# Optimization experiments

Measured on AMD Instinct MI355X. Metric: run time of the kernel, lower is better.

Reference implementation:

```python
import jax, jax.numpy as jnp
import numpy as np

NUM_HEADS = 16


def setup_inputs() -> dict:
    key = jax.random.key(0)
    ks = jax.random.split(key, 5)
    B, S, D = 2, 2048, 1024
    x = jax.random.normal(ks[0], (B, S, D), dtype=jnp.float32)
    # torch Linear weights are [out_features, in_features]; y = x @ W.T + b
    Wq = jax.random.normal(ks[1], (D, D), dtype=jnp.float32) * (D ** -0.5)
    Wk = jax.random.normal(ks[2], (D, D), dtype=jnp.float32) * (D ** -0.5)
    Wv = jax.random.normal(ks[3], (D, D), dtype=jnp.float32) * (D ** -0.5)
    Wo = jax.random.normal(ks[4], (D, D), dtype=jnp.float32) * (D ** -0.5)
    bo = jnp.zeros((D,), dtype=jnp.float32)
    return {"x": x, "Wq": Wq, "Wk": Wk, "Wv": Wv, "Wo": Wo, "bo": bo}


def reference(x, Wq, Wk, Wv, Wo, bo):
    B, S, D = x.shape
    H = NUM_HEADS
    dh = D // H
    # projections (torch Linear: x @ W.T)
    q = (x @ Wq.T).reshape(B, S, H, dh).transpose(0, 2, 1, 3)  # [B,H,S,dh]
    k = (x @ Wk.T).reshape(B, S, H, dh).transpose(0, 2, 1, 3)
    v = (x @ Wv.T).reshape(B, S, H, dh).transpose(0, 2, 1, 3)
    # NOTE: original code takes shape[-1] of the TRANSPOSED key (n,H,dh,S),
    # so the softmax scale is seq_length**-0.5 (a bug we reproduce faithfully).
    scale = jnp.asarray(S, x.dtype) ** -0.5
    scores = jnp.einsum("bhqd,bhkd->bhqk", q, k)  # [B,H,S,S]
    causal = jnp.triu(jnp.ones((S, S), dtype=bool), k=1)
    scores = jnp.where(causal, -jnp.inf, scores * scale)
    weights = jax.nn.softmax(scores, axis=-1)
    # dropout p=0.0 -> identity
    ctx = jnp.einsum("bhqk,bhkd->bhqd", weights, v)  # [B,H,S,dh]
    ctx = ctx.transpose(0, 2, 1, 3).reshape(B, S, D)
    return ctx @ Wo.T + bo
```

## Files before the change

kernel.cpp:

```cpp
#include <hip/hip_runtime.h>
#include <hip/hip_bf16.h>

#define B_SZ    2
#define S_LEN   2048
#define D_MODEL 1024
#define H_NUM   16
#define DH      64
#define M_TOT   (B_SZ * S_LEN)

#define QSCALE (0.022097086912079608f * 1.4426950408889634f)

typedef __attribute__((ext_vector_type(8)))  short          bf16x8;
typedef __attribute__((ext_vector_type(4)))  float          f32x4;
typedef __attribute__((ext_vector_type(16))) float          f32x16;
typedef __attribute__((ext_vector_type(8)))  unsigned short u16x8;
typedef __attribute__((ext_vector_type(4)))  unsigned short u16x4;

__device__ inline unsigned short f2bf(float f) {
  unsigned int u = __float_as_uint(f);
  u += 0x7fffu + ((u >> 16) & 1u);
  return (unsigned short)(u >> 16);
}

__device__ inline float bf2f(unsigned short u) {
  return __uint_as_float(((unsigned)u) << 16);
}

__device__ inline float fexp2(float x) {
#if __has_builtin(__builtin_amdgcn_exp2f)
  return __builtin_amdgcn_exp2f(x);
#else
  return exp2f(x);
#endif
}

__device__ inline unsigned cvt_pk_bf16(float lo, float hi) {
  unsigned r;
  asm("v_cvt_pk_bf16_f32 %0, %1, %2" : "=v"(r) : "v"(lo), "v"(hi));
  return r;
}

__device__ inline void gload16(const void* g, void* l) {
  __builtin_amdgcn_global_load_lds(
      (const __attribute__((address_space(1))) void*)g,
      (__attribute__((address_space(3))) void*)l, 16, 0, 0);
}

__global__ __launch_bounds__(256) void to_bf16_all(
    const float* __restrict__ x, const float* __restrict__ wq,
    const float* __restrict__ wk, const float* __restrict__ wv,
    const float* __restrict__ wo, unsigned short* __restrict__ xb,
    unsigned short* __restrict__ wqb, unsigned short* __restrict__ wkb,
    unsigned short* __restrict__ wvb, unsigned short* __restrict__ wob) {
  const size_t i = ((size_t)blockIdx.x * 256 + threadIdx.x) * 8;
  const float* src;
  unsigned short* dst;
  size_t off;
  if (i < 4194304)      { src = x;  dst = xb;  off = i; }
  else if (i < 5242880) { src = wq; dst = wqb; off = i - 4194304; }
  else if (i < 6291456) { src = wk; dst = wkb; off = i - 5242880; }
  else if (i < 7340032) { src = wv; dst = wvb; off = i - 6291456; }
  else                  { src = wo; dst = wob; off = i - 7340032; }
  f32x4 a = *(const f32x4*)(src + off);
  f32x4 b = *(const f32x4*)(src + off + 4);
  u16x8 o;
#pragma unroll
  for (int j = 0; j < 4; j++) { o[j] = f2bf(a[j]); o[4 + j] = f2bf(b[j]); }
  *(u16x8*)(dst + off) = o;
}

__device__ __forceinline__ void gemm_core(const unsigned short* __restrict__ A,
                                          const unsigned short* __restrict__ W,
                                          unsigned short (*Al)[128][32],
                                          unsigned short (*Bl)[128][32],
                                          int mbase, int nbase,
                                          f32x4 acc[4][4]) {
  const int tid  = threadIdx.x;
  const int lane = tid & 63;
  const int wid  = tid >> 6;
  const int wr   = wid >> 1, wc = wid & 1;
  const int g    = lane >> 4, lr = lane & 15;

  const int r0 = tid >> 2;
  const int cg = (tid & 3) ^ ((tid >> 3) & 3);

  const unsigned short* Abase = A + (size_t)(mbase + r0) * D_MODEL + cg * 8;
  const unsigned short* Wbase = W + (size_t)(nbase + r0) * D_MODEL + cg * 8;
  char* ldsA0 = (char*)Al + wid * 1024;
  char* ldsB0 = (char*)Bl + wid * 1024;

  gload16(Abase, ldsA0);
  gload16(Abase + (size_t)64 * D_MODEL, ldsA0 + 4096);
  gload16(Wbase, ldsB0);
  gload16(Wbase + (size_t)64 * D_MODEL, ldsB0 + 4096);
  gload16(Abase + 32, ldsA0 + 8192);
  gload16(Abase + (size_t)64 * D_MODEL + 32, ldsA0 + 8192 + 4096);
  gload16(Wbase + 32, ldsB0 + 8192);
  gload16(Wbase + (size_t)64 * D_MODEL + 32, ldsB0 + 8192 + 4096);

  const int NKT = D_MODEL / 32;
  int cur = 0, nx2 = 2;
  for (int kt = 0; kt < NKT; ++kt) {
    if (kt + 2 < NKT) {
      const unsigned short* As = Abase + (kt + 2) * 32;
      const unsigned short* Ws = Wbase + (kt + 2) * 32;
      char* la = ldsA0 + nx2 * 8192;
      char* lb = ldsB0 + nx2 * 8192;
      gload16(As, la);
      gload16(As + (size_t)64 * D_MODEL, la + 4096);
      gload16(Ws, lb);
      gload16(Ws + (size_t)64 * D_MODEL, lb + 4096);
      asm volatile("s_waitcnt vmcnt(8)" ::: "memory");
    } else if (kt + 1 < NKT) {
      asm volatile("s_waitcnt vmcnt(4)" ::: "memory");
    } else {
      asm volatile("s_waitcnt vmcnt(0)" ::: "memory");
    }
    __builtin_amdgcn_s_barrier();

    bf16x8 af[4], bfr[4];
#pragma unroll
    for (int i = 0; i < 4; i++) {
      const int ra = wr * 64 + i * 16 + lr;
      af[i] = *(const bf16x8*)&Al[cur][ra][(g ^ ((ra >> 1) & 3)) * 8];
      const int rb = wc * 64 + i * 16 + lr;
      bfr[i] = *(const bf16x8*)&Bl[cur][rb][(g ^ ((rb >> 1) & 3)) * 8];
    }
    __builtin_amdgcn_s_setprio(1);
#pragma unroll
    for (int i = 0; i < 4; i++)
#pragma unroll
      for (int j = 0; j < 4; j++)
        acc[i][j] = __builtin_amdgcn_mfma_f32_16x16x32_bf16(af[i], bfr[j],
                                                            acc[i][j], 0, 0, 0);
    __builtin_amdgcn_s_setprio(0);
    asm volatile("" ::: "memory");
    __builtin_amdgcn_s_barrier();
    cur = (cur == 2) ? 0 : cur + 1;
    nx2 = (nx2 == 2) ? 0 : nx2 + 1;
  }
}

__global__ __launch_bounds__(256) void gemm_qkv(
    const unsigned short* __restrict__ xb, const unsigned short* __restrict__ wqb,
    const unsigned short* __restrict__ wkb, const unsigned short* __restrict__ wvb,
    unsigned short* __restrict__ qb, unsigned short* __restrict__ kb,
    unsigned short* __restrict__ vt) {
  __shared__ unsigned short Al[3][128][32];
  __shared__ unsigned short Bl[3][128][32];
  const int lin = blockIdx.x;
  const int w8  = (lin & 7) * 96 + (lin >> 3);
  const int xq  = w8 & 7;
  const int yq  = (w8 >> 3) & 31;
  const int z   = w8 >> 8;
  const unsigned short* W = (z == 0) ? wqb : (z == 1) ? wkb : wvb;
  unsigned short* dst = (z == 0) ? qb : (z == 1) ? kb : vt;
  const float sc = (z == 0) ? QSCALE : 1.0f;

  f32x4 acc[4][4];
#pragma unroll
  for (int i = 0; i < 4; i++)
#pragma unroll
    for (int j = 0; j < 4; j++) acc[i][j] = (f32x4){0.f, 0.f, 0.f, 0.f};

  const int mbase = yq * 128, nbase = xq * 128;
  gemm_core(xb, W, Al, Bl, mbase, nbase, acc);

  const int lane = threadIdx.x & 63, wid = threadIdx.x >> 6;
  const int wr = wid >> 1, wc = wid & 1, g = lane >> 4, lr = lane & 15;
#pragma unroll
  for (int i = 0; i < 4; i++) {
#pragma unroll
    for (int j = 0; j < 4; j++) {
      const int mg0 = mbase + wr * 64 + i * 16 + g * 4;
      const int ng  = nbase + wc * 64 + j * 16 + lr;
      if (z < 2) {
#pragma unroll
        for (int r = 0; r < 4; r++)
          dst[(size_t)(mg0 + r) * D_MODEL + ng] = f2bf(acc[i][j][r] * sc);
      } else {
        const int hh = ng >> 6, dd = ng & 63;
        const int bb = mg0 >> 11, ss = mg0 & 2047;
        u16x4 pk;
#pragma unroll
        for (int r = 0; r < 4; r++) pk[r] = f2bf(acc[i][j][r]);
        *(u16x4*)&dst[((size_t)((bb * H_NUM + hh) * DH + dd)) * S_LEN + ss] = pk;
      }
    }
  }
}

__global__ __launch_bounds__(256) void gemm_out(
    const unsigned short* __restrict__ cx, const unsigned short* __restrict__ wob,
    float* __restrict__ out, const float* __restrict__ bo) {
  __shared__ unsigned short Al[3][128][32];
  __shared__ unsigned short Bl[3][128][32];
  const int lin = blockIdx.x;
  const int w8  = (lin & 7) * 32 + (lin >> 3);
  const int xq  = w8 & 7;
  const int yq  = w8 >> 3;
  f32x4 acc[4][4];
#pragma unroll
  for (int i = 0; i < 4; i++)
#pragma unroll
    for (int j = 0; j < 4; j++) acc[i][j] = (f32x4){0.f, 0.f, 0.f, 0.f};

  const int mbase = yq * 128, nbase = xq * 128;
  gemm_core(cx, wob, Al, Bl, mbase, nbase, acc);

  const int lane = threadIdx.x & 63, wid = threadIdx.x >> 6;
  const int wr = wid >> 1, wc = wid & 1, g = lane >> 4, lr = lane & 15;
#pragma unroll
  for (int i = 0; i < 4; i++) {
#pragma unroll
    for (int j = 0; j < 4; j++) {
      const int mg0 = mbase + wr * 64 + i * 16 + g * 4;
      const int ng  = nbase + wc * 64 + j * 16 + lr;
      const float bv = bo[ng];
#pragma unroll
      for (int r = 0; r < 4; r++)
        out[(size_t)(mg0 + r) * D_MODEL + ng] = acc[i][j][r] + bv;
    }
  }
}

#define ENT(qi, k0, k1, p) ((unsigned)(qi) | ((unsigned)(k0) << 8) | \
                            ((unsigned)(k1) << 16) | ((unsigned)(p) << 24))
__device__ const unsigned att_sched[40] = {
    ENT(3, 0, 8, 0),   ENT(7, 0, 8, 0),   ENT(7, 8, 16, 1),
    ENT(10, 0, 8, 0),  ENT(11, 0, 8, 0),  ENT(11, 8, 16, 1),
    ENT(11, 16, 24, 2),ENT(14, 0, 8, 0),  ENT(14, 15, 23, 2),
    ENT(15, 0, 8, 0),  ENT(15, 8, 16, 1), ENT(15, 16, 24, 2),
    ENT(15, 24, 32, 3),
    ENT(6, 0, 7, 0),   ENT(6, 7, 14, 1),  ENT(9, 0, 7, 0),
    ENT(9, 7, 14, 1),  ENT(10, 8, 15, 1), ENT(10, 15, 22, 2),
    ENT(12, 0, 7, 0),  ENT(12, 13, 20, 2),ENT(13, 0, 7, 0),
    ENT(13, 7, 14, 1), ENT(13, 14, 21, 2),ENT(13, 21, 28, 3),
    ENT(14, 8, 15, 1), ENT(14, 23, 30, 3),
    ENT(2, 0, 6, 0),   ENT(5, 0, 6, 0),   ENT(5, 6, 12, 1),
    ENT(8, 0, 6, 0),   ENT(8, 6, 12, 1),  ENT(8, 12, 18, 2),
    ENT(9, 14, 20, 2), ENT(12, 7, 13, 1), ENT(12, 20, 26, 3),
    ENT(4, 0, 5, 0),   ENT(4, 5, 10, 1),  ENT(1, 0, 4, 0),
    ENT(0, 0, 2, 0),
};
__device__ const int att_chunks[16]   = {1,1,1,1, 2,2,2,2, 3,3,3,3, 4,4,4,4};
__device__ const int att_mlbase[16]   = {0,1,2,3, 4,6,8,10, 12,15,18,21,
                                         24,28,32,36};
__device__ const int att_opbase[16]   = {0,0,0,0, 0,1,2,3, 4,6,8,10,
                                         12,15,18,21};

__global__ __launch_bounds__(256) void attn_v8(
    const unsigned short* __restrict__ qb, const unsigned short* __restrict__ kb,
    const unsigned short* __restrict__ vt, unsigned short* __restrict__ cx,
    unsigned short* __restrict__ Opart, float* __restrict__ ml) {
  __shared__ alignas(16) char smem[65536];

  const int tid  = threadIdx.x;
  const int lane = tid & 63;
  const int w    = tid >> 6;
  const int hi   = lane >> 5;
  const int lq   = lane & 31;
  const int bid  = blockIdx.x;

  const unsigned ent = att_sched[bid >> 5];
  const int qi   = ent & 255;
  const int kt0  = (ent >> 8) & 255;
  const int kt1  = (ent >> 16) & 255;
  const int part = (ent >> 24) & 255;
  const int nch  = att_chunks[qi];
  const int bh   = bid & 31;
  const int b    = bh >> 4, h = bh & 15;

  const int qg0  = qi * 128 + w * 32;
  const int tok0 = b * S_LEN + qg0;

  const int sr  = tid >> 3;
  const int scg = (tid & 7) ^ (sr & 7);
  const unsigned short* kbase =
      kb + (size_t)(b * S_LEN) * D_MODEL + h * DH + scg * 8;
  const unsigned short* vrow =
      vt + ((size_t)((b * H_NUM + h) * DH + sr)) * S_LEN + scg * 8;
  char* ldsK0 = smem + w * 1024;
  char* ldsV0 = smem + 32768 + w * 1024;

  bf16x8 qf[4];
  {
    const unsigned short* qrow =
        qb + (size_t)(tok0 + lq) * D_MODEL + h * DH + hi * 8;
#pragma unroll
    for (int ks = 0; ks < 4; ks++) qf[ks] = *(const bf16x8*)(qrow + ks * 16);
  }

  f32x16 ctx0, ctx1;
#pragma unroll
  for (int r = 0; r < 16; r++) { ctx0[r] = 0.f; ctx1[r] = 0.f; }
  float l_run = 0.f;

  const int ndiag = 2 * qi;

  {
    const unsigned short* sK = kbase + (size_t)(kt0 * 64 + sr) * D_MODEL;
    gload16(sK, ldsK0);
    gload16(sK + (size_t)32 * D_MODEL, ldsK0 + 4096);
    const unsigned short* sV = vrow + kt0 * 64;
    gload16(sV, ldsV0);
    gload16(sV + (size_t)32 * S_LEN, ldsV0 + 4096);
    if (kt0 + 1 < kt1) {
      const unsigned short* sK1 = sK + (size_t)64 * D_MODEL;
      gload16(sK1, ldsK0 + 8192);
      gload16(sK1 + (size_t)32 * D_MODEL, ldsK0 + 8192 + 4096);
      const unsigned short* sV1 = sV + 64;
      gload16(sV1, ldsV0 + 8192);
      gload16(sV1 + (size_t)32 * S_LEN, ldsV0 + 8192 + 4096);
    }
  }

  int cur = 0, nx2 = 2;
  for (int kt = kt0; kt < kt1; ++kt) {
    if (kt + 2 < kt1) {
      const unsigned short* sK = kbase + (size_t)((kt + 2) * 64 + sr) * D_MODEL;
      gload16(sK, ldsK0 + nx2 * 8192);
      gload16(sK + (size_t)32 * D_MODEL, ldsK0 + nx2 * 8192 + 4096);
      const unsigned short* sV = vrow + (kt + 2) * 64;
      gload16(sV, ldsV0 + nx2 * 8192);
      gload16(sV + (size_t)32 * S_LEN, ldsV0 + nx2 * 8192 + 4096);
      asm volatile("s_waitcnt vmcnt(8)" ::: "memory");
    } else if (kt + 1 < kt1) {
      asm volatile("s_waitcnt vmcnt(4)" ::: "memory");
    } else {
      asm volatile("s_waitcnt vmcnt(0)" ::: "memory");
    }
    __builtin_amdgcn_s_barrier();

    const char* Kc = smem + cur * 8192;
    const char* Vc = smem + 32768 + cur * 8192;

    f32x16 s0, s1;
#pragma unroll
    for (int r = 0; r < 16; r++) { s0[r] = 0.f; s1[r] = 0.f; }
    __builtin_amdgcn_s_setprio(1);
#pragma unroll
    for (int ks = 0; ks < 4; ks++) {
      const int c = ((ks * 2 + hi) ^ (lq & 7)) * 16;
      bf16x8 k0 = *(const bf16x8*)(Kc + lq * 128 + c);
      bf16x8 k1 = *(const bf16x8*)(Kc + (32 + lq) * 128 + c);
      s0 = __builtin_amdgcn_mfma_f32_32x32x16_bf16(k0, qf[ks], s0, 0, 0, 0);
      s1 = __builtin_amdgcn_mfma_f32_32x32x16_bf16(k1, qf[ks], s1, 0, 0, 0);
    }
    __builtin_amdgcn_s_setprio(0);

    if (kt >= ndiag) {
      const int relq = qg0 + lq - kt * 64 - 4 * hi;
#pragma unroll
      for (int r = 0; r < 16; r++) {
        const int ko = (r & 3) + 8 * (r >> 2);
        s0[r] = (ko > relq) ? -1e30f : s0[r];
        s1[r] = (ko + 32 > relq) ? -1e30f : s1[r];
      }
    }

    float lsAcc[4];
#pragma unroll
    for (int ks = 0; ks < 4; ks++) {
      float p[8];
#pragma unroll
      for (int j = 0; j < 8; j++) {
        const int r = (ks & 1) * 8 + j;
        const float sv = (ks < 2) ? s0[r] : s1[r];
        p[j] = fexp2(sv);
      }
      lsAcc[ks] = ((p[0] + p[1]) + (p[2] + p[3])) +
                  ((p[4] + p[5]) + (p[6] + p[7]));
      unsigned a0 = cvt_pk_bf16(p[0], p[1]);
      unsigned a1 = cvt_pk_bf16(p[4], p[5]);
      unsigned b0 = cvt_pk_bf16(p[2], p[3]);
      unsigned b1 = cvt_pk_bf16(p[6], p[7]);
      asm("v_permlane32_swap_b32 %0, %1" : "+v"(a0), "+v"(a1));
      asm("v_permlane32_swap_b32 %0, %1" : "+v"(b0), "+v"(b1));
      union { unsigned u[4]; bf16x8 v; } pw;
      pw.u[0] = a0;
      pw.u[1] = b0;
      pw.u[2] = a1;
      pw.u[3] = b1;
      const int c = ((ks * 2 + hi) ^ (lq & 7)) * 16;
      bf16x8 v0 = *(const bf16x8*)(Vc + lq * 128 + c);
      bf16x8 v1 = *(const bf16x8*)(Vc + (32 + lq) * 128 + c);
      __builtin_amdgcn_s_setprio(1);
      ctx0 = __builtin_amdgcn_mfma_f32_32x32x16_bf16(v0, pw.v, ctx0, 0, 0, 0);
      ctx1 = __builtin_amdgcn_mfma_f32_32x32x16_bf16(v1, pw.v, ctx1, 0, 0, 0);
      __builtin_amdgcn_s_setprio(0);
    }
    l_run += (lsAcc[0] + lsAcc[1]) + (lsAcc[2] + lsAcc[3]);
    cur = (cur + 1) & 3;
    nx2 = (nx2 + 1) & 3;
  }

  __builtin_amdgcn_s_barrier();
  unsigned short (*Tl)[32][72] = (unsigned short (*)[32][72])smem;
  const float lfull = l_run + __shfl_xor(l_run, 32);
  const float inv   = (nch == 1) ? (1.0f / lfull) : 1.0f;
#pragma unroll
  for (int rp = 0; rp < 8; rp++) {
    const int r  = rp * 2;
    const int d0 = (r & 3) + 8 * (r >> 2) + 4 * hi;
    *(unsigned*)&Tl[w][lq][d0] = cvt_pk_bf16(ctx0[r] * inv, ctx0[r + 1] * inv);
    *(unsigned*)&Tl[w][lq][32 + d0] =
        cvt_pk_bf16(ctx1[r] * inv, ctx1[r + 1] * inv);
  }
  asm volatile("s_waitcnt lgkmcnt(0)" ::: "memory");
  const int q2 = lane >> 1;
  unsigned short* dstp;
  if (nch == 1 || part == 0) {
    dstp = &cx[(size_t)(tok0 + q2) * D_MODEL + h * DH];
  } else {
    dstp = Opart + ((size_t)((att_opbase[qi] + part - 1) * 32 + bh) * 128 +
                    w * 32 + q2) * 64;
  }
#pragma unroll
  for (int i = 0; i < 4; i++) {
    const int ch = (lane & 1) * 4 + i;
    u16x8 vv = *(const u16x8*)&Tl[w][q2][ch * 8];
    *(u16x8*)&dstp[ch * 8] = vv;
  }
  if (nch > 1 && hi == 0) {
    float2 v2 = make_float2(0.0f, lfull);
    *(float2*)&ml[((size_t)((att_mlbase[qi] + part) * 32 + bh) * 128 +
                   w * 32 + lq) * 2] = v2;
  }
}

__global__ __launch_bounds__(256) void attn_combine(
    const unsigned short* __restrict__ Opart, const float* __restrict__ ml,
    unsigned short* __restrict__ cx) {
  const int gid = blockIdx.x * 256 + threadIdx.x;
  const int sub = gid & 7;
  const int row = (gid >> 3) & 127;
  const int bh  = (gid >> 10) & 31;
  const int qi  = 4 + (gid >> 15);
  const int nch = att_chunks[qi];
  const int b = bh >> 4, h = bh & 15;
  const int tok = b * S_LEN + qi * 128 + row;

  float mv[4], lv[4];
  float m = -1e30f;
#pragma unroll 4
  for (int p = 0; p < 4; p++) {
    if (p < nch) {
      const size_t mi =
          ((size_t)((att_mlbase[qi] + p) * 32 + bh) * 128 + row) * 2;
      mv[p] = ml[mi];
      lv[p] = ml[mi + 1];
      m = fmaxf(m, mv[p]);
    }
  }
  float denom = 0.f;
  float wgt[4];
#pragma unroll 4
  for (int p = 0; p < 4; p++) {
    if (p < nch) {
      wgt[p] = fexp2(mv[p] - m);
      denom += lv[p] * wgt[p];
    }
  }
  const float inv = 1.0f / denom;

  float acc[8];
  {
    u16x8 a = *(const u16x8*)&cx[(size_t)tok * D_MODEL + h * DH + sub * 8];
#pragma unroll
    for (int j = 0; j < 8; j++) acc[j] = bf2f(a[j]) * wgt[0];
  }
#pragma unroll 4
  for (int p = 1; p < 4; p++) {
    if (p < nch) {
      const unsigned short* src =
          Opart + ((size_t)((att_opbase[qi] + p - 1) * 32 + bh) * 128 + row) * 64;
      u16x8 a = *(const u16x8*)&src[sub * 8];
#pragma unroll
      for (int j = 0; j < 8; j++) acc[j] += bf2f(a[j]) * wgt[p];
    }
  }
  u16x8 o;
#pragma unroll
  for (int j = 0; j < 8; j++) o[j] = f2bf(acc[j] * inv);
  *(u16x8*)&cx[(size_t)tok * D_MODEL + h * DH + sub * 8] = o;
}

extern "C" void kernel_launch(void* const* d_in, const int* in_sizes, int n_in,
                              void* d_out, int out_size, void* d_ws,
                              size_t ws_size, hipStream_t stream) {
  const float* x  = (const float*)d_in[0];
  const float* Wq = (const float*)d_in[1];
  const float* Wk = (const float*)d_in[2];
  const float* Wv = (const float*)d_in[3];
  const float* Wo = (const float*)d_in[4];
  const float* bo = (const float*)d_in[5];
  float* out = (float*)d_out;

  unsigned short* xb  = (unsigned short*)d_ws;
  unsigned short* wqb = xb  + (size_t)M_TOT * D_MODEL;
  unsigned short* wkb = wqb + (size_t)D_MODEL * D_MODEL;
  unsigned short* wvb = wkb + (size_t)D_MODEL * D_MODEL;
  unsigned short* wob = wvb + (size_t)D_MODEL * D_MODEL;
  unsigned short* qb  = wob + (size_t)D_MODEL * D_MODEL;
  unsigned short* kb  = qb  + (size_t)M_TOT * D_MODEL;
  unsigned short* vt  = kb  + (size_t)M_TOT * D_MODEL;
  unsigned short* cx  = vt  + (size_t)M_TOT * D_MODEL;
  unsigned short* Opart = xb;
  float*          ml    = (float*)(xb + (size_t)768 * 8192);

  to_bf16_all<<<4096, 256, 0, stream>>>(x, Wq, Wk, Wv, Wo, xb, wqb, wkb, wvb,
                                        wob);
  gemm_qkv<<<dim3(768), 256, 0, stream>>>(xb, wqb, wkb, wvb, qb, kb, vt);
  attn_v8<<<dim3(1280), 256, 0, stream>>>(qb, kb, vt, cx, Opart, ml);
  attn_combine<<<dim3(1536), 256, 0, stream>>>(Opart, ml, cx);
  gemm_out<<<dim3(256), 256, 0, stream>>>(cx, wob, out, bo);
}
```

Baseline: 109.8 us.

## Widen attention blocks to 256 queries with 8 waves sharing K/V tiles

The attention kernel now processes 256 query rows per block using 512 threads (8 waves), up from 128 rows with 4 waves. Each staged K/V tile is therefore reused by twice as many waves, halving redundant global K/V loads. The split-K work schedule, chunk tables, per-wave diagonal index and the partial-output and ml buffer layouts are rebuilt for 256-row tiles. The combine kernel drops its exp2 max-rescaling, since the stored max is always zero, and simply sums partials and denominators. In exchange the grid shrinks to 640 larger blocks, which may leave compute units less evenly loaded and lowers occupancy per block.

```diff
diff --git a/kernel.cpp b/kernel.cpp
--- a/kernel.cpp
+++ b/kernel.cpp
@@ -226,30 +226,21 @@
 
 #define ENT(qi, k0, k1, p) ((unsigned)(qi) | ((unsigned)(k0) << 8) | \
                             ((unsigned)(k1) << 16) | ((unsigned)(p) << 24))
-__device__ const unsigned att_sched[40] = {
-    ENT(3, 0, 8, 0),   ENT(7, 0, 8, 0),   ENT(7, 8, 16, 1),
-    ENT(10, 0, 8, 0),  ENT(11, 0, 8, 0),  ENT(11, 8, 16, 1),
-    ENT(11, 16, 24, 2),ENT(14, 0, 8, 0),  ENT(14, 15, 23, 2),
-    ENT(15, 0, 8, 0),  ENT(15, 8, 16, 1), ENT(15, 16, 24, 2),
-    ENT(15, 24, 32, 3),
-    ENT(6, 0, 7, 0),   ENT(6, 7, 14, 1),  ENT(9, 0, 7, 0),
-    ENT(9, 7, 14, 1),  ENT(10, 8, 15, 1), ENT(10, 15, 22, 2),
-    ENT(12, 0, 7, 0),  ENT(12, 13, 20, 2),ENT(13, 0, 7, 0),
-    ENT(13, 7, 14, 1), ENT(13, 14, 21, 2),ENT(13, 21, 28, 3),
-    ENT(14, 8, 15, 1), ENT(14, 23, 30, 3),
-    ENT(2, 0, 6, 0),   ENT(5, 0, 6, 0),   ENT(5, 6, 12, 1),
-    ENT(8, 0, 6, 0),   ENT(8, 6, 12, 1),  ENT(8, 12, 18, 2),
-    ENT(9, 14, 20, 2), ENT(12, 7, 13, 1), ENT(12, 20, 26, 3),
-    ENT(4, 0, 5, 0),   ENT(4, 5, 10, 1),  ENT(1, 0, 4, 0),
-    ENT(0, 0, 2, 0),
+__device__ const unsigned att_sched[20] = {
+    ENT(1, 0, 8, 0),
+    ENT(3, 0, 8, 0),  ENT(3, 8, 16, 1),
+    ENT(5, 0, 8, 0),  ENT(5, 8, 16, 1),  ENT(5, 16, 24, 2),
+    ENT(7, 0, 8, 0),  ENT(7, 8, 16, 1),  ENT(7, 16, 24, 2), ENT(7, 24, 32, 3),
+    ENT(4, 0, 7, 0),  ENT(4, 7, 14, 1),
+    ENT(6, 0, 7, 0),  ENT(6, 7, 14, 1),  ENT(6, 14, 21, 2), ENT(6, 21, 28, 3),
+    ENT(2, 0, 6, 0),  ENT(2, 6, 12, 1),  ENT(4, 14, 20, 2),
+    ENT(0, 0, 4, 0),
 };
-__device__ const int att_chunks[16]   = {1,1,1,1, 2,2,2,2, 3,3,3,3, 4,4,4,4};
-__device__ const int att_mlbase[16]   = {0,1,2,3, 4,6,8,10, 12,15,18,21,
-                                         24,28,32,36};
-__device__ const int att_opbase[16]   = {0,0,0,0, 0,1,2,3, 4,6,8,10,
-                                         12,15,18,21};
-
-__global__ __launch_bounds__(256) void attn_v8(
+__device__ const int att_chunks[8] = {1, 1, 2, 2, 3, 3, 4, 4};
+__device__ const int att_mlbase[8] = {0, 1, 2, 4, 6, 9, 12, 16};
+__device__ const int att_opbase[8] = {0, 0, 0, 1, 2, 4, 6, 9};
+
+__global__ __launch_bounds__(512) void attn_v9(
     const unsigned short* __restrict__ qb, const unsigned short* __restrict__ kb,
     const unsigned short* __restrict__ vt, unsigned short* __restrict__ cx,
     unsigned short* __restrict__ Opart, float* __restrict__ ml) {
@@ -271,7 +262,7 @@
   const int bh   = bid & 31;
   const int b    = bh >> 4, h = bh & 15;
 
-  const int qg0  = qi * 128 + w * 32;
+  const int qg0  = qi * 256 + w * 32;
   const int tok0 = b * S_LEN + qg0;
 
   const int sr  = tid >> 3;
@@ -296,37 +287,24 @@
   for (int r = 0; r < 16; r++) { ctx0[r] = 0.f; ctx1[r] = 0.f; }
   float l_run = 0.f;
 
-  const int ndiag = 2 * qi;
+  const int ndiag = 4 * qi + (w >> 1);
 
   {
-    const unsigned short* sK = kbase + (size_t)(kt0 * 64 + sr) * D_MODEL;
-    gload16(sK, ldsK0);
-    gload16(sK + (size_t)32 * D_MODEL, ldsK0 + 4096);
-    const unsigned short* sV = vrow + kt0 * 64;
-    gload16(sV, ldsV0);
-    gload16(sV + (size_t)32 * S_LEN, ldsV0 + 4096);
-    if (kt0 + 1 < kt1) {
-      const unsigned short* sK1 = sK + (size_t)64 * D_MODEL;
-      gload16(sK1, ldsK0 + 8192);
-      gload16(sK1 + (size_t)32 * D_MODEL, ldsK0 + 8192 + 4096);
-      const unsigned short* sV1 = sV + 64;
-      gload16(sV1, ldsV0 + 8192);
-      gload16(sV1 + (size_t)32 * S_LEN, ldsV0 + 8192 + 4096);
-    }
+    gload16(kbase + (size_t)(kt0 * 64 + sr) * D_MODEL, ldsK0);
+    gload16(vrow + kt0 * 64, ldsV0);
+    gload16(kbase + (size_t)((kt0 + 1) * 64 + sr) * D_MODEL, ldsK0 + 8192);
+    gload16(vrow + (kt0 + 1) * 64, ldsV0 + 8192);
   }
 
   int cur = 0, nx2 = 2;
   for (int kt = kt0; kt < kt1; ++kt) {
     if (kt + 2 < kt1) {
-      const unsigned short* sK = kbase + (size_t)((kt + 2) * 64 + sr) * D_MODEL;
-      gload16(sK, ldsK0 + nx2 * 8192);
-      gload16(sK + (size_t)32 * D_MODEL, ldsK0 + nx2 * 8192 + 4096);
-      const unsigned short* sV = vrow + (kt + 2) * 64;
-      gload16(sV, ldsV0 + nx2 * 8192);
-      gload16(sV + (size_t)32 * S_LEN, ldsV0 + nx2 * 8192 + 4096);
-      asm volatile("s_waitcnt vmcnt(8)" ::: "memory");
+      gload16(kbase + (size_t)((kt + 2) * 64 + sr) * D_MODEL,
+              ldsK0 + nx2 * 8192);
+      gload16(vrow + (kt + 2) * 64, ldsV0 + nx2 * 8192);
+      asm volatile("s_waitcnt vmcnt(4)" ::: "memory");
     } else if (kt + 1 < kt1) {
-      asm volatile("s_waitcnt vmcnt(4)" ::: "memory");
+      asm volatile("s_waitcnt vmcnt(2)" ::: "memory");
     } else {
       asm volatile("s_waitcnt vmcnt(0)" ::: "memory");
     }
@@ -413,7 +391,7 @@
   if (nch == 1 || part == 0) {
     dstp = &cx[(size_t)(tok0 + q2) * D_MODEL + h * DH];
   } else {
-    dstp = Opart + ((size_t)((att_opbase[qi] + part - 1) * 32 + bh) * 128 +
+    dstp = Opart + ((size_t)((att_opbase[qi] + part - 1) * 32 + bh) * 256 +
                     w * 32 + q2) * 64;
   }
 #pragma unroll
@@ -424,7 +402,7 @@
   }
   if (nch > 1 && hi == 0) {
     float2 v2 = make_float2(0.0f, lfull);
-    *(float2*)&ml[((size_t)((att_mlbase[qi] + part) * 32 + bh) * 128 +
+    *(float2*)&ml[((size_t)((att_mlbase[qi] + part) * 32 + bh) * 256 +
                    w * 32 + lq) * 2] = v2;
   }
 }
@@ -434,50 +412,43 @@
     unsigned short* __restrict__ cx) {
   const int gid = blockIdx.x * 256 + threadIdx.x;
   const int sub = gid & 7;
-  const int row = (gid >> 3) & 127;
-  const int bh  = (gid >> 10) & 31;
-  const int qi  = 4 + (gid >> 15);
+  const int row = (gid >> 3) & 255;
+  const int bh  = (gid >> 11) & 31;
+  const int qi  = 2 + (gid >> 16);
   const int nch = att_chunks[qi];
   const int b = bh >> 4, h = bh & 15;
-  const int tok = b * S_LEN + qi * 128 + row;
-
-  float mv[4], lv[4];
-  float m = -1e30f;
+  const int tok = b * S_LEN + qi * 256 + row;
+
+  float lv[4];
 #pragma unroll 4
   for (int p = 0; p < 4; p++) {
     if (p < nch) {
       const size_t mi =
-          ((size_t)((att_mlbase[qi] + p) * 32 + bh) * 128 + row) * 2;
-      mv[p] = ml[mi];
+          ((size_t)((att_mlbase[qi] + p) * 32 + bh) * 256 + row) * 2;
       lv[p] = ml[mi + 1];
-      m = fmaxf(m, mv[p]);
     }
   }
   float denom = 0.f;
-  float wgt[4];
 #pragma unroll 4
-  for (int p = 0; p < 4; p++) {
-    if (p < nch) {
-      wgt[p] = fexp2(mv[p] - m);
-      denom += lv[p] * wgt[p];
-    }
-  }
+  for (int p = 0; p < 4; p++)
+    if (p < nch) denom += lv[p];
   const float inv = 1.0f / denom;
 
   float acc[8];
   {
     u16x8 a = *(const u16x8*)&cx[(size_t)tok * D_MODEL + h * DH + sub * 8];
 #pragma unroll
-    for (int j = 0; j < 8; j++) acc[j] = bf2f(a[j]) * wgt[0];
+    for (int j = 0; j < 8; j++) acc[j] = bf2f(a[j]);
   }
 #pragma unroll 4
   for (int p = 1; p < 4; p++) {
     if (p < nch) {
       const unsigned short* src =
-          Opart + ((size_t)((att_opbase[qi] + p - 1) * 32 + bh) * 128 + row) * 64;
+          Opart +
+          ((size_t)((att_opbase[qi] + p - 1) * 32 + bh) * 256 + row) * 64;
       u16x8 a = *(const u16x8*)&src[sub * 8];
 #pragma unroll
-      for (int j = 0; j < 8; j++) acc[j] += bf2f(a[j]) * wgt[p];
+      for (int j = 0; j < 8; j++) acc[j] += bf2f(a[j]);
     }
   }
   u16x8 o;
@@ -507,12 +478,12 @@
   unsigned short* vt  = kb  + (size_t)M_TOT * D_MODEL;
   unsigned short* cx  = vt  + (size_t)M_TOT * D_MODEL;
   unsigned short* Opart = xb;
-  float*          ml    = (float*)(xb + (size_t)768 * 8192);
+  float*          ml    = (float*)(xb + (size_t)12 * 32 * 256 * 64);
 
   to_bf16_all<<<4096, 256, 0, stream>>>(x, Wq, Wk, Wv, Wo, xb, wqb, wkb, wvb,
                                         wob);
   gemm_qkv<<<dim3(768), 256, 0, stream>>>(xb, wqb, wkb, wvb, qb, kb, vt);
-  attn_v8<<<dim3(1280), 256, 0, stream>>>(qb, kb, vt, cx, Opart, ml);
+  attn_v9<<<dim3(640), 512, 0, stream>>>(qb, kb, vt, cx, Opart, ml);
   attn_combine<<<dim3(1536), 256, 0, stream>>>(Opart, ml, cx);
   gemm_out<<<dim3(256), 256, 0, stream>>>(cx, wob, out, bo);
 }
```

Result: slower. 112.3 us (+2.3%).
